# Kernel tuning notes

Hardware: AMD Instinct MI355X
Metric: run time of the kernel (lower is better)

## Reference

```python
import jax, jax.numpy as jnp
import numpy as np

DIM = 2048
HEADS = 32
DIM_HEAD = 64
FF_INNER = DIM * 4
SCALE_BASE = 512
FUSED = HEADS * DIM_HEAD + DIM_HEAD + DIM_HEAD + FF_INNER * 2  # 18560


def setup_inputs() -> dict:
    key = jax.random.key(0)
    k1, k2, k3, k4 = jax.random.split(key, 4)
    b, n = 2, 2048
    x = jax.random.normal(k1, (b, n, DIM), dtype=jnp.float32)
    W_fused = jax.random.normal(k2, (FUSED, DIM), dtype=jnp.float32) * 0.02
    W_attn_out = jax.random.normal(k3, (DIM, HEADS * DIM_HEAD), dtype=jnp.float32) * 0.02
    W_ff_out = jax.random.normal(k4, (DIM, FF_INNER), dtype=jnp.float32) * 0.02
    gamma = jnp.ones((DIM,), dtype=jnp.float32)
    return {"x": x, "gamma": gamma, "W_fused": W_fused,
            "W_attn_out": W_attn_out, "W_ff_out": W_ff_out}


def _rotate_half(t):
    t1, t2 = jnp.split(t, 2, axis=-1)
    return jnp.concatenate((-t2, t1), axis=-1)


def _rotary(n, dtype):
    # xpos rotary embeddings: freqs [n, dim_head], scale [n, dim_head]
    inv_freq = 1.0 / (10000.0 ** (jnp.arange(0, DIM_HEAD, 2, dtype=jnp.float32) / DIM_HEAD))
    t = jnp.arange(n, dtype=jnp.float32)
    freqs = t[:, None] * inv_freq[None, :]
    freqs = jnp.concatenate((freqs, freqs), axis=-1)
    power = (t - n // 2) / SCALE_BASE
    scale_base_vec = (jnp.arange(0, DIM_HEAD, 2, dtype=jnp.float32) + 0.4 * DIM_HEAD) / (1.4 * DIM_HEAD)
    scale = scale_base_vec[None, :] ** power[:, None]
    scale = jnp.concatenate((scale, scale), axis=-1)
    return freqs.astype(dtype), scale.astype(dtype)


def _apply_rotary(pos, t, scale):
    return t * jnp.cos(pos) * scale + _rotate_half(t) * jnp.sin(pos) * scale


def reference(x, gamma, W_fused, W_attn_out, W_ff_out):
    b, n, d = x.shape
    # LayerNorm (beta fixed at zero)
    mu = jnp.mean(x, axis=-1, keepdims=True)
    var = jnp.mean((x - mu) ** 2, axis=-1, keepdims=True)
    xn = (x - mu) * jax.lax.rsqrt(var + 1e-5) * gamma

    # fused QKV + FF projection
    proj = jnp.einsum('bnd,fd->bnf', xn, W_fused)
    attn_inner = HEADS * DIM_HEAD
    q = proj[..., :attn_inner]
    k = proj[..., attn_inner:attn_inner + DIM_HEAD]
    v = proj[..., attn_inner + DIM_HEAD:attn_inner + 2 * DIM_HEAD]
    ff = proj[..., attn_inner + 2 * DIM_HEAD:]

    # multi-query attention with xpos rotary
    q = q.reshape(b, n, HEADS, DIM_HEAD).transpose(0, 2, 1, 3)  # b h n d
    q = q * (DIM_HEAD ** -0.5)
    pos, scale = _rotary(n, x.dtype)
    q = _apply_rotary(pos, q, scale)          # broadcasts over b,h
    k = _apply_rotary(pos, k, 1.0 / scale)    # k is [b, n, dim_head]

    sim = jnp.einsum('bhid,bjd->bhij', q, k)
    causal_mask = jnp.triu(jnp.ones((n, n), dtype=bool), k=1)
    sim = jnp.where(causal_mask, -jnp.finfo(sim.dtype).max, sim)
    attn = jax.nn.softmax(sim, axis=-1)
    out = jnp.einsum('bhij,bjd->bhid', attn, v)
    out = out.transpose(0, 2, 1, 3).reshape(b, n, attn_inner)
    attn_out = jnp.einsum('bnf,df->bnd', out, W_attn_out)

    # SwiGLU FF
    ff_x, gate = jnp.split(ff, 2, axis=-1)
    ff_hidden = jax.nn.silu(gate) * ff_x
    ff_out = jnp.einsum('bnf,df->bnd', ff_hidden, W_ff_out)

    return attn_out + ff_out
```

## Files before the change

kernel.cpp:

```cpp
#include <hip/hip_runtime.h>
#include <cstdint>
#include <cstddef>

typedef __bf16 bf16;
typedef float f32x4 __attribute__((ext_vector_type(4)));
typedef bf16  bf16x4 __attribute__((ext_vector_type(4)));
typedef bf16  bf16x8 __attribute__((ext_vector_type(8)));

#define DIMD   2048
#define HEADS  32
#define DH     64
#define FFI    8192
#define FUSEDN 18560
#define FUSEDP 18688
#define BB     2
#define NN     2048
#define MROWS  4096
#define K2     10240

__device__ __forceinline__ void gl_lds16(const void* g, void* l) {
  __builtin_amdgcn_global_load_lds(
      (__attribute__((address_space(1))) void*)const_cast<void*>(g),
      (__attribute__((address_space(3))) void*)l, 16, 0, 0);
}

__device__ __forceinline__ void nt_store_bf16(bf16 v, bf16* p) {
  union { bf16 b; short s; } u; u.b = v;
  __builtin_nontemporal_store(u.s, (short*)p);
}

template <int THREADS>
__device__ __forceinline__ void stage_i(const bf16* g, long ldk,
                                        bf16* region, int instr, int tid) {
  int row = instr * (THREADS / 8) + (tid >> 3);
  int cs  = (tid & 7) ^ (row & 7);
  gl_lds16(g + (size_t)row * ldk + cs * 8,
           region + (size_t)instr * (THREADS * 8) + (size_t)(tid & ~63) * 8);
}

struct SrcT { const bf16* g; long ldk; };

template <typename FA, typename FB>
__device__ __forceinline__ void gemm_2ph(FA fa, FB fb, const int NT,
    bf16* As, bf16* Bs, f32x4 (&acc)[4][4],
    const int tid, const int wrow, const int nbase, const int l15, const int h4)
{
  const char* aP[2]; const char* bP[2];
  const int arow = wrow + l15, brow = nbase + l15;
#pragma unroll
  for (int ks = 0; ks < 2; ks++) {
    aP[ks] = (const char*)As + arow * 128 + (((ks * 4 + h4) ^ (arow & 7)) * 16);
    bP[ks] = (const char*)Bs + brow * 128 + (((ks * 4 + h4) ^ (brow & 7)) * 16);
  }
  for (int t = 0; t < NT; ++t) {
    __syncthreads();
    {
      auto a = fa(t); auto b = fb(t);
#pragma unroll
      for (int q = 0; q < 4; q++) stage_i<256>(a.g, a.ldk, As, q, tid);
#pragma unroll
      for (int q = 0; q < 4; q++) stage_i<256>(b.g, b.ldk, Bs, q, tid);
    }
    __syncthreads();
#pragma unroll
    for (int ks = 0; ks < 2; ks++) {
      bf16x8 af[4], bfr[4];
#pragma unroll
      for (int m_ = 0; m_ < 4; m_++) af[m_]  = *(const bf16x8*)(aP[ks] + m_ * 2048);
#pragma unroll
      for (int n_ = 0; n_ < 4; n_++) bfr[n_] = *(const bf16x8*)(bP[ks] + n_ * 2048);
#pragma unroll
      for (int m_ = 0; m_ < 4; m_++)
#pragma unroll
        for (int n_ = 0; n_ < 4; n_++)
          acc[m_][n_] = __builtin_amdgcn_mfma_f32_16x16x32_bf16(af[m_], bfr[n_], acc[m_][n_], 0, 0, 0);
    }
  }
}

__global__ void k_cvt_flat(const float* __restrict__ s, bf16* __restrict__ d, long total8) {
  long stride = (long)gridDim.x * blockDim.x;
  for (long i = (long)blockIdx.x * blockDim.x + threadIdx.x; i < total8; i += stride) {
    long e = i << 3;
    float4 v0 = *(const float4*)(s + e);
    float4 v1 = *(const float4*)(s + e + 4);
    bf16x8 o;
    o[0]=(bf16)v0.x; o[1]=(bf16)v0.y; o[2]=(bf16)v0.z; o[3]=(bf16)v0.w;
    o[4]=(bf16)v1.x; o[5]=(bf16)v1.y; o[6]=(bf16)v1.z; o[7]=(bf16)v1.w;
    *(bf16x8*)(d + e) = o;
  }
}

__global__ void k_cvt_str8(const float* __restrict__ s, bf16* __restrict__ d,
                           long total8, int colshift, int dstride, int doff) {
  long stride = (long)gridDim.x * blockDim.x;
  for (long i = (long)blockIdx.x * blockDim.x + threadIdx.x; i < total8; i += stride) {
    long e = i << 3;
    long r = e >> colshift;
    int  c = (int)(e & ((1L << colshift) - 1));
    float4 v0 = *(const float4*)(s + e);
    float4 v1 = *(const float4*)(s + e + 4);
    bf16x8 o;
    o[0]=(bf16)v0.x; o[1]=(bf16)v0.y; o[2]=(bf16)v0.z; o[3]=(bf16)v0.w;
    o[4]=(bf16)v1.x; o[5]=(bf16)v1.y; o[6]=(bf16)v1.z; o[7]=(bf16)v1.w;
    *(bf16x8*)(d + r * (long)dstride + doff + c) = o;
  }
}

__global__ __launch_bounds__(256) void k_ln(const float* __restrict__ x,
                                            const float* __restrict__ g,
                                            bf16* __restrict__ xn) {
  int row = blockIdx.x, t = threadIdx.x;
  const float4* xr = (const float4*)(x + (size_t)row * DIMD);
  float4 a = xr[t*2], b = xr[t*2+1];
  float s  = a.x+a.y+a.z+a.w + b.x+b.y+b.z+b.w;
  float s2 = a.x*a.x+a.y*a.y+a.z*a.z+a.w*a.w + b.x*b.x+b.y*b.y+b.z*b.z+b.w*b.w;
  for (int o = 1; o < 64; o <<= 1) { s += __shfl_xor(s, o); s2 += __shfl_xor(s2, o); }
  __shared__ float rs[8];
  if ((t & 63) == 0) { rs[t>>6] = s; rs[4 + (t>>6)] = s2; }
  __syncthreads();
  s = rs[0]+rs[1]+rs[2]+rs[3]; s2 = rs[4]+rs[5]+rs[6]+rs[7];
  float mu = s * (1.f/DIMD);
  float var = s2 * (1.f/DIMD) - mu*mu;
  float rstd = rsqrtf(var + 1e-5f);
  const float4* gr = (const float4*)g;
  float4 g0 = gr[t*2], g1 = gr[t*2+1];
  bf16x8 o;
  o[0]=(bf16)((a.x-mu)*rstd*g0.x); o[1]=(bf16)((a.y-mu)*rstd*g0.y);
  o[2]=(bf16)((a.z-mu)*rstd*g0.z); o[3]=(bf16)((a.w-mu)*rstd*g0.w);
  o[4]=(bf16)((b.x-mu)*rstd*g1.x); o[5]=(bf16)((b.y-mu)*rstd*g1.y);
  o[6]=(bf16)((b.z-mu)*rstd*g1.z); o[7]=(bf16)((b.w-mu)*rstd*g1.w);
  *(bf16x8*)(xn + (size_t)row * DIMD + t*8) = o;
}

__global__ __launch_bounds__(256, 3) void k_gemm1(const bf16* __restrict__ xn,
                                                  const bf16* __restrict__ wf,
                                                  bf16* __restrict__ q_raw,
                                                  bf16* __restrict__ k_buf,
                                                  bf16* __restrict__ v_t,
                                                  bf16* __restrict__ proj_ff) {
  __shared__ bf16 As[128*64];
  __shared__ bf16 Bs[128*64];
  const int tid = threadIdx.x, w = tid >> 6, l = tid & 63;
  const int l15 = l & 15, h4 = l >> 4;
  const int wrow = (w >> 1) * 64, nbase = (w & 1) * 64;
  const int bid = blockIdx.x;
  const int bs = (bid & 7) * 584 + (bid >> 3);
  const int mt = bs / 146, nt = bs - mt * 146;
  const int m0 = mt * 128, f0 = nt * 128;

  f32x4 acc[4][4];
#pragma unroll
  for (int i = 0; i < 4; i++)
#pragma unroll
    for (int j = 0; j < 4; j++) acc[i][j] = (f32x4){0.f,0.f,0.f,0.f};

  auto fa = [&](int t) -> SrcT { return SrcT{ xn + (size_t)m0 * DIMD + t * 64, (long)DIMD }; };
  auto fb = [&](int t) -> SrcT { return SrcT{ wf + (size_t)f0 * DIMD + t * 64, (long)DIMD }; };
  gemm_2ph(fa, fb, DIMD / 64, As, Bs, acc, tid, wrow, nbase, l15, h4);

#pragma unroll
  for (int m_ = 0; m_ < 4; m_++)
#pragma unroll
    for (int nf = 0; nf < 4; nf++) {
      int fcol = f0 + nbase + nf*16 + l15;
      if (fcol < FUSEDN) {
#pragma unroll
        for (int j = 0; j < 4; j++) {
          int m = m0 + wrow + m_*16 + h4*4 + j;
          bf16 bv = (bf16)acc[m_][nf][j];
          int b = m >> 11, n = m & 2047;
          if (fcol < 2048) {
            int hh = fcol >> 6, d = fcol & 63;
            q_raw[(((size_t)(b*HEADS + hh) * NN + n) << 6) + d] = bv;
          } else if (fcol < 2112) {
            k_buf[(((size_t)(b*NN + n)) << 6) + (fcol - 2048)] = bv;
          } else if (fcol < 2176) {
            v_t[(((size_t)(b*DH + (fcol - 2112))) << 11) + n] = bv;
          } else {
            nt_store_bf16(bv, proj_ff + ((size_t)m << 14) + (fcol - 2176));
          }
        }
      }
    }
}

__global__ __launch_bounds__(256, 3) void k_gemm2(const bf16* __restrict__ u_o,
                                                  const bf16* __restrict__ ffh,
                                                  const bf16* __restrict__ wcat,
                                                  float* __restrict__ out,
                                                  float* __restrict__ part) {
  __shared__ bf16 As[128*64];
  __shared__ bf16 Bs[128*64];
  const int tid = threadIdx.x, w = tid >> 6, l = tid & 63;
  const int l15 = l & 15, h4 = l >> 4;
  const int wrow = (w >> 1) * 64, nbase = (w & 1) * 64;
  const int bid = blockIdx.x;
  const int kk = bid >> 9;
  const int inner = bid & 511;
  const int bs = (inner & 7) * 64 + (inner >> 3);
  const int mt = bs >> 4, nt = bs & 15;
  const int m0 = mt * 128, f0 = nt * 128;
  const int T0 = kk * 80;

  f32x4 acc[4][4];
#pragma unroll
  for (int i = 0; i < 4; i++)
#pragma unroll
    for (int j = 0; j < 4; j++) acc[i][j] = (f32x4){0.f,0.f,0.f,0.f};

  auto fa = [&](int t) -> SrcT {
    int tt = t + T0;
    if (tt < 32) return SrcT{ u_o + (size_t)m0 * DIMD + tt * 64, (long)DIMD };
    return SrcT{ ffh + (size_t)m0 * 16384 + (tt - 32) * 64, (long)16384 };
  };
  auto fb = [&](int t) -> SrcT { return SrcT{ wcat + (size_t)f0 * K2 + (t + T0) * 64, (long)K2 }; };
  gemm_2ph(fa, fb, 80, As, Bs, acc, tid, wrow, nbase, l15, h4);

  float* dst = kk ? part : out;
#pragma unroll
  for (int m_ = 0; m_ < 4; m_++)
#pragma unroll
    for (int nf = 0; nf < 4; nf++) {
      int fcol = f0 + nbase + nf*16 + l15;
#pragma unroll
      for (int j = 0; j < 4; j++) {
        int m = m0 + wrow + m_*16 + h4*4 + j;
        __builtin_nontemporal_store(acc[m_][nf][j], dst + (size_t)m * DIMD + fcol);
      }
    }
}

__global__ void k_addout(float* __restrict__ out, const float* __restrict__ part, long total4) {
  long stride = (long)gridDim.x * blockDim.x;
  for (long i = (long)blockIdx.x * blockDim.x + threadIdx.x; i < total4; i += stride) {
    long e = i << 2;
    float4 a = *(const float4*)(out + e);
    float4 b = *(const float4*)(part + e);
    float4 r; r.x = a.x + b.x; r.y = a.y + b.y; r.z = a.z + b.z; r.w = a.w + b.w;
    *(float4*)(out + e) = r;
  }
}

__global__ void k_rope(bf16* __restrict__ q_raw, bf16* __restrict__ k_buf) {
  const long QT = (long)BB*HEADS*NN*32;
  const long TOT = QT + (long)BB*NN*32;
  long gid = (long)blockIdx.x * blockDim.x + threadIdx.x;
  if (gid >= TOT) return;
  bool isq = gid < QT;
  long idx = isq ? gid : gid - QT;
  int  i = (int)(idx & 31);
  long row = idx >> 5;
  int  n = (int)(row & (NN - 1));
  bf16* base = (isq ? q_raw : k_buf) + row * DH;
  float t1 = (float)base[i];
  float t2 = (float)base[i + 32];
  float inv_freq = exp2f((float)i * -0.4152410118f);
  float th = (float)n * inv_freq;
  float sn, cs;
  __sincosf(th, &sn, &cs);
  float power = ((float)n - (float)(NN/2)) * (1.f/512.f);
  float sb = ((float)(2*i) + 25.6f) * (1.f/89.6f);
  float sc = exp2f((isq ? power : -power) * __log2f(sb));
  float mm = isq ? 0.125f : 1.0f;
  float o1 = (t1*cs - t2*sn) * sc * mm;
  float o2 = (t2*cs + t1*sn) * sc * mm;
  base[i]      = (bf16)o1;
  base[i + 32] = (bf16)o2;
}

__global__ __launch_bounds__(256) void k_attn(const bf16* __restrict__ qbuf,
                                              const bf16* __restrict__ kbuf,
                                              const bf16* __restrict__ vtb,
                                              bf16* __restrict__ uo) {
  __shared__ bf16 Qs[128*64];
  __shared__ bf16 Ks[32*64];
  __shared__ bf16 Vs[64*32];
  const int tid = threadIdx.x, w = tid >> 6, l = tid & 63;
  const int l15 = l & 15, h4 = l >> 4;
  const int bid = blockIdx.x;
  const int qt = 15 - (bid & 15);
  const int bh = bid >> 4;
  const int h = bh & (HEADS - 1), b = bh >> 5;
  const int q0 = qt * 128;
  const bf16* Qg = qbuf + ((size_t)(b*HEADS + h) * NN + q0) * DH;
  const bf16* Kg = kbuf + (size_t)b * NN * DH;
  const bf16* Vg = vtb + (size_t)b * DH * NN;

#pragma unroll
  for (int c = 0; c < 4; c++) {
    int chunk = c*256 + tid;
    int r = chunk >> 3, cc = chunk & 7;
    int col8 = (cc ^ (r & 7)) << 3;
    gl_lds16(Qg + (size_t)r*DH + col8, Qs + ((size_t)(chunk & ~63) << 3));
  }
  __syncthreads();

  const int wq0 = q0 + w*32;
  bf16x8 qfr[2][2];
#pragma unroll
  for (int qf = 0; qf < 2; qf++)
#pragma unroll
    for (int c = 0; c < 2; c++) {
      int row = w*32 + qf*16 + l15;
      int x = (64*c + 16*h4) ^ (16*(row & 7));
      qfr[qf][c] = *(const bf16x8*)((const char*)Qs + row*128 + x);
    }

  f32x4 zf = {0.f,0.f,0.f,0.f};
  f32x4 o_[2][4];
#pragma unroll
  for (int qf = 0; qf < 2; qf++)
#pragma unroll
    for (int nf = 0; nf < 4; nf++) o_[qf][nf] = zf;
  float mrun[2] = {-3e38f, -3e38f};
  float lrun[2] = {0.f, 0.f};

  const int nsteps = (q0 + 128) >> 5;
  for (int kt = 0; kt < nsteps; kt++) {
    const int kv0 = kt << 5;
    {
      int r = tid >> 3, cc = tid & 7;
      int col8 = (cc ^ (r & 7)) << 3;
      gl_lds16(Kg + (size_t)(kv0 + r)*DH + col8, Ks + ((size_t)(tid & ~63) << 3));
    }
    {
      int d = tid >> 2, cc = tid & 3;
      int col8 = (cc ^ (d & 3)) << 3;
      gl_lds16(Vg + (size_t)d*NN + kv0 + col8, Vs + ((size_t)(tid & ~63) << 3));
    }
    __syncthreads();
    if (kv0 <= wq0 + 31) {
      bf16x8 ka[2][2];
#pragma unroll
      for (int kvf = 0; kvf < 2; kvf++)
#pragma unroll
        for (int c = 0; c < 2; c++) {
          int r = kvf*16 + l15;
          int x = (64*c + 16*h4) ^ (16*(r & 7));
          ka[kvf][c] = *(const bf16x8*)((const char*)Ks + r*128 + x);
        }
      f32x4 st[2][2];
#pragma unroll
      for (int kvf = 0; kvf < 2; kvf++)
#pragma unroll
        for (int qf = 0; qf < 2; qf++) {
          f32x4 s = __builtin_amdgcn_mfma_f32_16x16x32_bf16(ka[kvf][0], qfr[qf][0], zf, 0, 0, 0);
          s = __builtin_amdgcn_mfma_f32_16x16x32_bf16(ka[kvf][1], qfr[qf][1], s, 0, 0, 0);
          st[kvf][qf] = s;
        }
      if (kv0 + 31 > wq0) {
#pragma unroll
        for (int kvf = 0; kvf < 2; kvf++)
#pragma unroll
          for (int j = 0; j < 4; j++) {
            int kvg = kv0 + kvf*16 + h4*4 + j;
#pragma unroll
            for (int qf = 0; qf < 2; qf++) {
              int qg = wq0 + qf*16 + l15;
              if (kvg > qg) st[kvf][qf][j] = -3e38f;
            }
          }
      }
      bf16x8 pa[2];
#pragma unroll
      for (int qf = 0; qf < 2; qf++) {
        float vmax = -3e38f;
#pragma unroll
        for (int kvf = 0; kvf < 2; kvf++)
#pragma unroll
          for (int j = 0; j < 4; j++) vmax = fmaxf(vmax, st[kvf][qf][j]);
        vmax = fmaxf(vmax, __shfl_xor(vmax, 16));
        vmax = fmaxf(vmax, __shfl_xor(vmax, 32));
        float mnew = fmaxf(mrun[qf], vmax);
        float corr = __expf(mrun[qf] - mnew);
        float ps = 0.f;
        float pv_[8];
#pragma unroll
        for (int kvf = 0; kvf < 2; kvf++)
#pragma unroll
          for (int j = 0; j < 4; j++) {
            float p = __expf(st[kvf][qf][j] - mnew);
            pv_[kvf*4 + j] = p; ps += p;
          }
        ps += __shfl_xor(ps, 16);
        ps += __shfl_xor(ps, 32);
        lrun[qf] = lrun[qf]*corr + ps;
        mrun[qf] = mnew;
        bf16x8 t;
#pragma unroll
        for (int i = 0; i < 8; i++) t[i] = (bf16)pv_[i];
        pa[qf] = t;
#pragma unroll
        for (int j = 0; j < 4; j++) {
          float cj = __shfl(corr, (l & 48) | (h4*4 + j), 64);
#pragma unroll
          for (int nf = 0; nf < 4; nf++) o_[qf][nf][j] *= cj;
        }
      }
#pragma unroll
      for (int nf = 0; nf < 4; nf++) {
        int d_ = nf*16 + l15;
        int swz = 16*(d_ & 3);
        const char* vrow = (const char*)Vs + d_*64;
        bf16x4 v0 = *(const bf16x4*)(vrow + ((8*h4) ^ swz));
        bf16x4 v1 = *(const bf16x4*)(vrow + ((8*h4 + 32) ^ swz));
        bf16x8 vb = __builtin_shufflevector(v0, v1, 0,1,2,3,4,5,6,7);
#pragma unroll
        for (int qf = 0; qf < 2; qf++)
          o_[qf][nf] = __builtin_amdgcn_mfma_f32_16x16x32_bf16(pa[qf], vb, o_[qf][nf], 0, 0, 0);
      }
    }
    __syncthreads();
  }
#pragma unroll
  for (int qf = 0; qf < 2; qf++) {
    float inv = 1.f / lrun[qf];
#pragma unroll
    for (int j = 0; j < 4; j++) {
      float ij = __shfl(inv, (l & 48) | (h4*4 + j), 64);
      int qg = wq0 + qf*16 + h4*4 + j;
      size_t rowoff = (size_t)(b*NN + qg) * DIMD + h*DH;
#pragma unroll
      for (int nf = 0; nf < 4; nf++)
        uo[rowoff + nf*16 + l15] = (bf16)(o_[qf][nf][j] * ij);
    }
  }
}

__global__ void k_silu(bf16* __restrict__ pf) {
  const long total4 = (long)MROWS * FFI / 4;
  long stride = (long)gridDim.x * blockDim.x;
  for (long i = (long)blockIdx.x * blockDim.x + threadIdx.x; i < total4; i += stride) {
    long e = i << 2;
    long m = e >> 13;
    int  c = (int)(e & (FFI - 1));
    bf16* px = pf + (m << 14) + c;
    bf16x4 fx = *(const bf16x4*)px;
    bf16x4 gt = *(const bf16x4*)(px + FFI);
    bf16x4 r;
#pragma unroll
    for (int k = 0; k < 4; k++) {
      float g = (float)gt[k], f = (float)fx[k];
      float s = g * (1.f / (1.f + __expf(-g)));
      r[k] = (bf16)(s * f);
    }
    *(bf16x4*)px = r;
  }
}

extern "C" void kernel_launch(void* const* d_in, const int* in_sizes, int n_in,
                              void* d_out, int out_size, void* d_ws, size_t ws_size,
                              hipStream_t stream) {
  const float* x     = (const float*)d_in[0];
  const float* gamma = (const float*)d_in[1];
  const float* Wf    = (const float*)d_in[2];
  const float* Wao   = (const float*)d_in[3];
  const float* Wff   = (const float*)d_in[4];
  float* out = (float*)d_out;
  char* ws = (char*)d_ws;

  size_t o = 0;
  bf16* wfb     = (bf16*)(ws + o); o += (size_t)FUSEDP * DIMD * 2;
  bf16* wcat    = wfb;
  bf16* xn      = (bf16*)(ws + o); o += (size_t)MROWS * DIMD * 2;
  bf16* q_raw   = (bf16*)(ws + o); o += (size_t)BB*HEADS*NN*DH * 2;
  bf16* k_buf   = (bf16*)(ws + o); o += (size_t)BB*NN*DH * 2;
  bf16* v_t     = (bf16*)(ws + o); o += (size_t)BB*DH*NN * 2;
  bf16* proj_ff = (bf16*)(ws + o); o += (size_t)MROWS * 2*FFI * 2;
  bf16* u_o     = (bf16*)(ws + o); o += (size_t)MROWS * DIMD * 2;
  float* part   = (float*)xn;

  k_cvt_flat<<<2048, 256, 0, stream>>>(Wf, wfb, (long)FUSEDN*DIMD/8);
  k_ln<<<MROWS, 256, 0, stream>>>(x, gamma, xn);
  k_gemm1<<<(FUSEDP/128)*(MROWS/128), 256, 0, stream>>>(xn, wfb, q_raw, k_buf, v_t, proj_ff);
  k_cvt_str8<<<512,  256, 0, stream>>>(Wao, wcat, (long)DIMD*DIMD/8, 11, K2, 0);
  k_cvt_str8<<<1024, 256, 0, stream>>>(Wff, wcat, (long)DIMD*FFI/8,  13, K2, DIMD);
  {
    long tot = (long)BB*HEADS*NN*32 + (long)BB*NN*32;
    k_rope<<<(int)((tot + 255) / 256), 256, 0, stream>>>(q_raw, k_buf);
  }
  k_attn<<<BB*HEADS*(NN/128), 256, 0, stream>>>(q_raw, k_buf, v_t, u_o);
  k_silu<<<2048, 256, 0, stream>>>(proj_ff);
  k_gemm2<<<2*(MROWS/128)*(DIMD/128), 256, 0, stream>>>(u_o, proj_ff, wcat, out, part);
  k_addout<<<2048, 256, 0, stream>>>(out, part, (long)MROWS*DIMD/4);
}
```

Measured before the change: 852.3 us.

## Fuse SwiGLU into projection GEMM epilogue via interleaved weight permutation

Permutes the FF rows of the fused weight during bf16 conversion so that each 64-column warp tile holds 32 value columns and their matching 32 gate columns. The GEMM1 epilogue can then compute silu(gate)*x in registers and write a half-width ffh buffer. This removes the separate silu kernel and the write and re-read of the full 2*FFI projection. It also changes GEMM2 output stores from nontemporal to regular stores.

```diff
diff --git a/kernel.cpp b/kernel.cpp
--- a/kernel.cpp
+++ b/kernel.cpp
@@ -24,11 +24,6 @@
       (__attribute__((address_space(3))) void*)l, 16, 0, 0);
 }
 
-__device__ __forceinline__ void nt_store_bf16(bf16 v, bf16* p) {
-  union { bf16 b; short s; } u; u.b = v;
-  __builtin_nontemporal_store(u.s, (short*)p);
-}
-
 template <int THREADS>
 __device__ __forceinline__ void stage_i(const bf16* g, long ldk,
                                         bf16* region, int instr, int tid) {
@@ -78,16 +73,25 @@
   }
 }
 
-__global__ void k_cvt_flat(const float* __restrict__ s, bf16* __restrict__ d, long total8) {
+__global__ void k_cvt_perm(const float* __restrict__ s, bf16* __restrict__ d, long total8) {
   long stride = (long)gridDim.x * blockDim.x;
   for (long i = (long)blockIdx.x * blockDim.x + threadIdx.x; i < total8; i += stride) {
     long e = i << 3;
-    float4 v0 = *(const float4*)(s + e);
-    float4 v1 = *(const float4*)(s + e + 4);
-    bf16x8 o;
-    o[0]=(bf16)v0.x; o[1]=(bf16)v0.y; o[2]=(bf16)v0.z; o[3]=(bf16)v0.w;
-    o[4]=(bf16)v1.x; o[5]=(bf16)v1.y; o[6]=(bf16)v1.z; o[7]=(bf16)v1.w;
-    *(bf16x8*)(d + e) = o;
+    int p = (int)(e >> 11);
+    int c = (int)(e & 2047);
+    int orig;
+    if (p < 2176) orig = p;
+    else {
+      int q = p - 2176, g = q >> 6, o = q & 63;
+      orig = (o < 32) ? (2176 + g * 32 + o) : (2176 + 8192 + g * 32 + (o - 32));
+    }
+    const float* src = s + (size_t)orig * 2048 + c;
+    float4 v0 = *(const float4*)src;
+    float4 v1 = *(const float4*)(src + 4);
+    bf16x8 o8;
+    o8[0]=(bf16)v0.x; o8[1]=(bf16)v0.y; o8[2]=(bf16)v0.z; o8[3]=(bf16)v0.w;
+    o8[4]=(bf16)v1.x; o8[5]=(bf16)v1.y; o8[6]=(bf16)v1.z; o8[7]=(bf16)v1.w;
+    *(bf16x8*)(d + e) = o8;
   }
 }
 
@@ -138,7 +142,7 @@
                                                   bf16* __restrict__ q_raw,
                                                   bf16* __restrict__ k_buf,
                                                   bf16* __restrict__ v_t,
-                                                  bf16* __restrict__ proj_ff) {
+                                                  bf16* __restrict__ ffh) {
   __shared__ bf16 As[128*64];
   __shared__ bf16 Bs[128*64];
   const int tid = threadIdx.x, w = tid >> 6, l = tid & 63;
@@ -159,12 +163,12 @@
   auto fb = [&](int t) -> SrcT { return SrcT{ wf + (size_t)f0 * DIMD + t * 64, (long)DIMD }; };
   gemm_2ph(fa, fb, DIMD / 64, As, Bs, acc, tid, wrow, nbase, l15, h4);
 
-#pragma unroll
-  for (int m_ = 0; m_ < 4; m_++)
-#pragma unroll
-    for (int nf = 0; nf < 4; nf++) {
-      int fcol = f0 + nbase + nf*16 + l15;
-      if (fcol < FUSEDN) {
+  if (nt < 17) {
+#pragma unroll
+    for (int m_ = 0; m_ < 4; m_++)
+#pragma unroll
+      for (int nf = 0; nf < 4; nf++) {
+        int fcol = f0 + nbase + nf*16 + l15;
 #pragma unroll
         for (int j = 0; j < 4; j++) {
           int m = m0 + wrow + m_*16 + h4*4 + j;
@@ -177,12 +181,29 @@
             k_buf[(((size_t)(b*NN + n)) << 6) + (fcol - 2048)] = bv;
           } else if (fcol < 2176) {
             v_t[(((size_t)(b*DH + (fcol - 2112))) << 11) + n] = bv;
-          } else {
-            nt_store_bf16(bv, proj_ff + ((size_t)m << 14) + (fcol - 2176));
           }
         }
       }
-    }
+  } else {
+    int base = f0 + nbase;
+    if (base < FUSEDN) {
+      int g = (base - 2176) >> 6;
+#pragma unroll
+      for (int m_ = 0; m_ < 4; m_++)
+#pragma unroll
+        for (int nf = 0; nf < 2; nf++) {
+          int xc = g*32 + nf*16 + l15;
+#pragma unroll
+          for (int j = 0; j < 4; j++) {
+            int m = m0 + wrow + m_*16 + h4*4 + j;
+            float xv = acc[m_][nf][j];
+            float gv = acc[m_][nf+2][j];
+            float sv = gv * (1.f / (1.f + __expf(-gv)));
+            ffh[((size_t)m << 13) + xc] = (bf16)(sv * xv);
+          }
+        }
+    }
+  }
 }
 
 __global__ __launch_bounds__(256, 3) void k_gemm2(const bf16* __restrict__ u_o,
@@ -212,7 +233,7 @@
   auto fa = [&](int t) -> SrcT {
     int tt = t + T0;
     if (tt < 32) return SrcT{ u_o + (size_t)m0 * DIMD + tt * 64, (long)DIMD };
-    return SrcT{ ffh + (size_t)m0 * 16384 + (tt - 32) * 64, (long)16384 };
+    return SrcT{ ffh + (size_t)m0 * FFI + (tt - 32) * 64, (long)FFI };
   };
   auto fb = [&](int t) -> SrcT { return SrcT{ wcat + (size_t)f0 * K2 + (t + T0) * 64, (long)K2 }; };
   gemm_2ph(fa, fb, 80, As, Bs, acc, tid, wrow, nbase, l15, h4);
@@ -226,7 +247,7 @@
 #pragma unroll
       for (int j = 0; j < 4; j++) {
         int m = m0 + wrow + m_*16 + h4*4 + j;
-        __builtin_nontemporal_store(acc[m_][nf][j], dst + (size_t)m * DIMD + fcol);
+        dst[(size_t)m * DIMD + fcol] = acc[m_][nf][j];
       }
     }
 }
@@ -428,27 +449,6 @@
   }
 }
 
-__global__ void k_silu(bf16* __restrict__ pf) {
-  const long total4 = (long)MROWS * FFI / 4;
-  long stride = (long)gridDim.x * blockDim.x;
-  for (long i = (long)blockIdx.x * blockDim.x + threadIdx.x; i < total4; i += stride) {
-    long e = i << 2;
-    long m = e >> 13;
-    int  c = (int)(e & (FFI - 1));
-    bf16* px = pf + (m << 14) + c;
-    bf16x4 fx = *(const bf16x4*)px;
-    bf16x4 gt = *(const bf16x4*)(px + FFI);
-    bf16x4 r;
-#pragma unroll
-    for (int k = 0; k < 4; k++) {
-      float g = (float)gt[k], f = (float)fx[k];
-      float s = g * (1.f / (1.f + __expf(-g)));
-      r[k] = (bf16)(s * f);
-    }
-    *(bf16x4*)px = r;
-  }
-}
-
 extern "C" void kernel_launch(void* const* d_in, const int* in_sizes, int n_in,
                               void* d_out, int out_size, void* d_ws, size_t ws_size,
                               hipStream_t stream) {
@@ -467,13 +467,13 @@
   bf16* q_raw   = (bf16*)(ws + o); o += (size_t)BB*HEADS*NN*DH * 2;
   bf16* k_buf   = (bf16*)(ws + o); o += (size_t)BB*NN*DH * 2;
   bf16* v_t     = (bf16*)(ws + o); o += (size_t)BB*DH*NN * 2;
-  bf16* proj_ff = (bf16*)(ws + o); o += (size_t)MROWS * 2*FFI * 2;
+  bf16* ffh     = (bf16*)(ws + o); o += (size_t)MROWS * FFI * 2;
   bf16* u_o     = (bf16*)(ws + o); o += (size_t)MROWS * DIMD * 2;
   float* part   = (float*)xn;
 
-  k_cvt_flat<<<2048, 256, 0, stream>>>(Wf, wfb, (long)FUSEDN*DIMD/8);
+  k_cvt_perm<<<2048, 256, 0, stream>>>(Wf, wfb, (long)FUSEDN*DIMD/8);
   k_ln<<<MROWS, 256, 0, stream>>>(x, gamma, xn);
-  k_gemm1<<<(FUSEDP/128)*(MROWS/128), 256, 0, stream>>>(xn, wfb, q_raw, k_buf, v_t, proj_ff);
+  k_gemm1<<<(FUSEDP/128)*(MROWS/128), 256, 0, stream>>>(xn, wfb, q_raw, k_buf, v_t, ffh);
   k_cvt_str8<<<512,  256, 0, stream>>>(Wao, wcat, (long)DIMD*DIMD/8, 11, K2, 0);
   k_cvt_str8<<<1024, 256, 0, stream>>>(Wff, wcat, (long)DIMD*FFI/8,  13, K2, DIMD);
   {
@@ -481,7 +481,6 @@
     k_rope<<<(int)((tot + 255) / 256), 256, 0, stream>>>(q_raw, k_buf);
   }
   k_attn<<<BB*HEADS*(NN/128), 256, 0, stream>>>(q_raw, k_buf, v_t, u_o);
-  k_silu<<<2048, 256, 0, stream>>>(proj_ff);
-  k_gemm2<<<2*(MROWS/128)*(DIMD/128), 256, 0, stream>>>(u_o, proj_ff, wcat, out, part);
+  k_gemm2<<<2*(MROWS/128)*(DIMD/128), 256, 0, stream>>>(u_o, ffh, wcat, out, part);
   k_addout<<<2048, 256, 0, stream>>>(out, part, (long)MROWS*DIMD/4);
 }
```

Measured after the change: 799.2 us. 6.2% less time.
